# Kernel optimization log

Measured on AMD Instinct MI355X. Metric: run time of the kernel, lower is better.

Reference implementation:

```python
import jax, jax.numpy as jnp
import numpy as np

NEG = -1e9  # sentinel for masked/assigned entries (fp32-safe)


def _greedy_max_connect(logits, mask_dec, mask_tgt):
    """Iterative greedy max-connect matching (previous_max_connect_search).

    Each round, every unassigned query row claims its best available target
    column; conflicts on a column are won by the highest-logit row. Winners
    are fixed and removed, and the process repeats until all valid rows are
    matched (or no columns remain). Returns (index [B,Q] int32,
    one_hot [B,Q,T] float, iter count).
    """
    B, Q, T = logits.shape
    valid = mask_dec[:, :, None] & mask_tgt[:, None, :]
    base = jnp.where(valid, logits, NEG)
    col_ids = jnp.arange(T, dtype=jnp.int32)
    row_ids = jnp.arange(Q, dtype=jnp.int32)

    def cond(state):
        row_done, col_done, assigned, index, it = state
        return jnp.logical_and(jnp.any(~row_done), it < Q)

    def body(state):
        row_done, col_done, assigned, index, it = state
        # mask out finished rows / taken columns
        scores = jnp.where(row_done[:, :, None] | col_done[:, None, :], NEG, base)  # [B,Q,T]
        best_val = jnp.max(scores, axis=-1)                      # [B,Q]
        best_col = jnp.argmax(scores, axis=-1).astype(jnp.int32)  # [B,Q]
        claiming = (~row_done) & (best_val > NEG / 2)
        # claim[b,q,t] = best_val if row q claims col t else NEG
        claim = jnp.where(
            claiming[:, :, None] & (best_col[:, :, None] == col_ids[None, None, :]),
            best_val[:, :, None], NEG)                           # [B,Q,T]
        win_row = jnp.argmax(claim, axis=1).astype(jnp.int32)    # [B,T]
        col_hit = jnp.max(claim, axis=1) > NEG / 2               # [B,T]
        row_wins = (claiming
                    & (jnp.take_along_axis(win_row, best_col, axis=1) == row_ids[None, :])
                    & jnp.take_along_axis(col_hit, best_col, axis=1))  # [B,Q]
        index = jnp.where(row_wins, best_col, index)
        assigned = assigned | row_wins
        # rows with no available column left are retired (stuck)
        row_done = row_done | row_wins | (best_val <= NEG / 2)
        col_done = col_done | col_hit
        return row_done, col_done, assigned, index, it + 1

    init = (~mask_dec, ~mask_tgt,
            jnp.zeros((B, Q), bool), jnp.zeros((B, Q), jnp.int32),
            jnp.array(0, jnp.int32))
    row_done, col_done, assigned, index, it = jax.lax.while_loop(cond, body, init)
    one_hot = (assigned[:, :, None]
               & (index[:, :, None] == col_ids[None, None, :])).astype(logits.dtype)
    return index, one_hot, it


def setup_inputs() -> dict:
    key = jax.random.key(0)
    k1, k2 = jax.random.split(key)
    B, Q, T, D = 4, 2048, 2048, 512
    return {
        "dec": jax.random.normal(k1, (B, Q, D), jnp.float32),
        "tgt": jax.random.normal(k2, (B, T, D), jnp.float32),
        "mask_dec": jnp.ones((B, Q), dtype=bool),
        "mask_tgt": jnp.ones((B, T), dtype=bool),
    }


def reference(dec, tgt, mask_dec, mask_tgt):
    # search_type=0, decompose=False -> inputs = dec, targets = tgt
    # normalize=True -> cosine-style logits (note: torch uses plain norm, no eps)
    inputs = dec / jnp.linalg.norm(dec, axis=-1, keepdims=True)
    targets = tgt / jnp.linalg.norm(tgt, axis=-1, keepdims=True)
    logits = jnp.einsum("bqd,btd->bqt", inputs, targets)  # [B,Q,T]
    index, one_hot, iters = _greedy_max_connect(logits, mask_dec, mask_tgt)
    return logits, index, one_hot, iters
```

## Files before the change

kernel.cpp:

```cpp
#include <hip/hip_runtime.h>

#define B_ 4
#define Q_ 2048
#define T_ 2048
#define D_ 512
#define K_ 16

typedef __attribute__((ext_vector_type(8))) __bf16 bf16x8;
typedef __attribute__((ext_vector_type(4))) float f32x4;

__device__ inline unsigned int fmap(float v) {
  unsigned int b = __float_as_uint(v);
  return (b & 0x80000000u) ? ~b : (b | 0x80000000u);
}

__device__ inline unsigned long long shfl_xor64(unsigned long long v, int m) {
  int lo = __shfl_xor((int)(unsigned int)(v & 0xFFFFFFFFULL), m, 64);
  int hi = __shfl_xor((int)(unsigned int)(v >> 32), m, 64);
  return ((unsigned long long)(unsigned int)hi << 32) | (unsigned int)lo;
}

__global__ __launch_bounds__(256) void convert_kernel(const float* __restrict__ dec,
                                                      const float* __restrict__ tgt,
                                                      __bf16* __restrict__ planes,
                                                      float* __restrict__ rq,
                                                      float* __restrict__ rt,
                                                      int* __restrict__ g_iters) {
  if (blockIdx.x == 0 && threadIdx.x == 0) g_iters[0] = 0;
  const int NR = B_ * Q_;
  int w = (blockIdx.x * blockDim.x + threadIdx.x) >> 6;
  int lane = threadIdx.x & 63;
  const bool isA = (w < NR);
  const int row = isA ? w : w - NR;
  const float* src = (isA ? dec : tgt) + (size_t)row * D_;

  float4 u = *(const float4*)(src + lane * 8);
  float4 v = *(const float4*)(src + lane * 8 + 4);
  float xs[8] = {u.x, u.y, u.z, u.w, v.x, v.y, v.z, v.w};

  bf16x8 h0, h1, h2;
  float s = 0.f;
#pragma unroll
  for (int j = 0; j < 8; ++j) {
    float x = xs[j];
    s += x * x;
    __bf16 a0 = (__bf16)x;
    float r1 = x - (float)a0;
    __bf16 a1 = (__bf16)r1;
    float r2 = r1 - (float)a1;
    __bf16 a2 = (__bf16)r2;
    h0[j] = a0; h1[j] = a1; h2[j] = a2;
  }
  const size_t PS = (size_t)NR * D_;
  __bf16* p = planes + (isA ? 0 : 3) * PS + (size_t)row * D_ + lane * 8;
  *(bf16x8*)(p)          = h0;
  *(bf16x8*)(p + PS)     = h1;
  *(bf16x8*)(p + 2 * PS) = h2;

#pragma unroll
  for (int off = 32; off; off >>= 1) s += __shfl_xor(s, off, 64);
  if (lane == 0) {
    float r = 1.0f / sqrtf(s);
    (isA ? rq : rt)[row] = r;
  }
}

__global__ __launch_bounds__(256) void gemm_kernel(const __bf16* __restrict__ planes,
                                                   const float* __restrict__ rq,
                                                   const float* __restrict__ rt,
                                                   float* __restrict__ C) {
  __shared__ __bf16 sA[3][128][40];
  __shared__ __bf16 sB[3][128][40];

  const size_t PS = (size_t)(B_ * Q_) * D_;
  const int bz = blockIdx.z;
  const int qb = blockIdx.y * 128, tb = blockIdx.x * 128;
  const int arow0 = bz * Q_ + qb;
  const int brow0 = bz * T_ + tb;
  const int t = threadIdx.x;
  const int lane = t & 63, wid = t >> 6;
  const int wr = wid >> 1, wc = wid & 1;
  const int fr = lane & 15;
  const int fg = lane >> 4;

  const __bf16* pA[3] = {planes, planes + PS, planes + 2 * PS};
  const __bf16* pB[3] = {planes + 3 * PS, planes + 4 * PS, planes + 5 * PS};

  f32x4 acc[4][4];
#pragma unroll
  for (int i = 0; i < 4; ++i)
#pragma unroll
    for (int j = 0; j < 4; ++j) acc[i][j] = (f32x4){0.f, 0.f, 0.f, 0.f};

  for (int ks = 0; ks < D_ / 32; ++ks) {
    const int k0 = ks * 32;
    __syncthreads();
#pragma unroll
    for (int p = 0; p < 3; ++p) {
#pragma unroll
      for (int i = 0; i < 2; ++i) {
        int c = t + i * 256;
        int row = c >> 2;
        int off = (c & 3) * 8;
        uint4 va = *(const uint4*)(pA[p] + (size_t)(arow0 + row) * D_ + k0 + off);
        *(uint4*)&sA[p][row][off] = va;
        uint4 vb = *(const uint4*)(pB[p] + (size_t)(brow0 + row) * D_ + k0 + off);
        *(uint4*)&sB[p][row][off] = vb;
      }
    }
    __syncthreads();

    bf16x8 bfr[4][3];
#pragma unroll
    for (int nt = 0; nt < 4; ++nt)
#pragma unroll
      for (int p = 0; p < 3; ++p)
        bfr[nt][p] = *(const bf16x8*)&sB[p][wc * 64 + nt * 16 + fr][fg * 8];

#pragma unroll
    for (int mt = 0; mt < 4; ++mt) {
      bf16x8 afr[3];
#pragma unroll
      for (int p = 0; p < 3; ++p)
        afr[p] = *(const bf16x8*)&sA[p][wr * 64 + mt * 16 + fr][fg * 8];
#pragma unroll
      for (int nt = 0; nt < 4; ++nt) {
        f32x4 c = acc[mt][nt];
        c = __builtin_amdgcn_mfma_f32_16x16x32_bf16(afr[0], bfr[nt][0], c, 0, 0, 0);
        c = __builtin_amdgcn_mfma_f32_16x16x32_bf16(afr[0], bfr[nt][1], c, 0, 0, 0);
        c = __builtin_amdgcn_mfma_f32_16x16x32_bf16(afr[1], bfr[nt][0], c, 0, 0, 0);
        c = __builtin_amdgcn_mfma_f32_16x16x32_bf16(afr[0], bfr[nt][2], c, 0, 0, 0);
        c = __builtin_amdgcn_mfma_f32_16x16x32_bf16(afr[1], bfr[nt][1], c, 0, 0, 0);
        c = __builtin_amdgcn_mfma_f32_16x16x32_bf16(afr[2], bfr[nt][0], c, 0, 0, 0);
        acc[mt][nt] = c;
      }
    }
  }

#pragma unroll
  for (int mt = 0; mt < 4; ++mt) {
    int q = qb + wr * 64 + mt * 16 + fg * 4;
    float rq0 = rq[bz * Q_ + q + 0];
    float rq1 = rq[bz * Q_ + q + 1];
    float rq2 = rq[bz * Q_ + q + 2];
    float rq3 = rq[bz * Q_ + q + 3];
#pragma unroll
    for (int nt = 0; nt < 4; ++nt) {
      int tc = tb + wc * 64 + nt * 16 + fr;
      float rtv = rt[bz * T_ + tc];
      float* cp = C + ((size_t)(bz * Q_ + q)) * T_ + tc;
      cp[0]          = acc[mt][nt][0] * rq0 * rtv;
      cp[T_]         = acc[mt][nt][1] * rq1 * rtv;
      cp[2 * (size_t)T_] = acc[mt][nt][2] * rq2 * rtv;
      cp[3 * (size_t)T_] = acc[mt][nt][3] * rq3 * rtv;
    }
  }
}

__global__ __launch_bounds__(256) void topk_kernel(const float* __restrict__ logits,
                                                   unsigned long long* __restrict__ cand) {
  int w = (blockIdx.x * blockDim.x + threadIdx.x) >> 6;
  int lane = threadIdx.x & 63;
  if (w >= B_ * Q_) return;
  const float* lp = logits + (size_t)w * T_;
  const int c0 = lane << 2;

  unsigned int v[32];
#pragma unroll
  for (int j = 0; j < 8; ++j) {
    float4 x = *(const float4*)(lp + j * 256 + c0);
    v[4 * j + 0] = fmap(x.x);
    v[4 * j + 1] = fmap(x.y);
    v[4 * j + 2] = fmap(x.z);
    v[4 * j + 3] = fmap(x.w);
  }

  unsigned int validmask = 0xFFFFFFFFu;
  unsigned int lm = 0u;
  int lj = 0;
#pragma unroll
  for (int j = 0; j < 32; ++j) {
    bool t = v[j] > lm;
    lm = t ? v[j] : lm;
    lj = t ? j : lj;
  }
  int lc = c0 + ((lj >> 2) << 8) + (lj & 3);

  unsigned long long mine = 0ULL;
#pragma unroll 1
  for (int it = 0; it < K_; ++it) {
    unsigned long long key = ((unsigned long long)lm << 32) | (unsigned int)~lc;
    unsigned long long wmax = key;
#pragma unroll
    for (int off = 32; off; off >>= 1) {
      unsigned long long o = shfl_xor64(wmax, off);
      if (o > wmax) wmax = o;
    }
    if (lane == it) mine = wmax;
    if (key == wmax) {
      validmask &= ~(1u << lj);
      lm = 0u; lj = 0;
#pragma unroll
      for (int j = 0; j < 32; ++j) {
        bool ok = (((validmask >> j) & 1u) != 0u) && (v[j] > lm);
        lm = ok ? v[j] : lm;
        lj = ok ? j : lj;
      }
      lc = c0 + ((lj >> 2) << 8) + (lj & 3);
    }
  }
  if (lane < K_) cand[(size_t)w * K_ + lane] = mine;
}

__global__ __launch_bounds__(1024) void match_kernel(const float* __restrict__ logits,
                                                     unsigned long long* __restrict__ cand,
                                                     int* __restrict__ g_index,
                                                     int* __restrict__ g_assigned,
                                                     int* __restrict__ g_iters) {
  __shared__ unsigned long long claim[T_];
  __shared__ unsigned char col_done[T_];
  __shared__ short bestc[Q_];
  __shared__ short queue[Q_];
  __shared__ short freelist[T_];
  __shared__ int qn, nfree_s, live_s;

  const int b = blockIdx.x;
  const int bq0 = b << 11;
  const int tid = threadIdx.x;
  const int lane = tid & 63, wid = tid >> 6;
  const int q0 = tid, q1 = tid + 1024;
  const unsigned long long lmask_lt = (1ULL << lane) - 1ULL;
  const unsigned int tagA = (unsigned int)~(unsigned int)q0;
  const unsigned int tagB = (unsigned int)~(unsigned int)q1;

  for (int i = tid; i < Q_; i += 1024) {
    claim[i] = 0ULL; col_done[i] = 0;
    g_index[bq0 + i] = 0; g_assigned[bq0 + i] = 0;
  }
  if (tid == 0) { qn = 0; live_s = Q_; }

  bool doneA = false, doneB = false;
  int cpA = 0, cpB = 0;
  unsigned long long ecA = cand[((size_t)(bq0 + q0)) * K_];
  unsigned long long ecB = cand[((size_t)(bq0 + q1)) * K_];

  int r = 0;
  for (;;) {
    __syncthreads();
    if (*(volatile int*)&live_s == 0 || r >= Q_) break;
    if (tid == 0) nfree_s = 0;

    bool clA = false, clB = false, quA = false, quB = false;
    int mcA = -1, mcB = -1;

    if (!doneA) {
      const unsigned long long* cp = cand + ((size_t)(bq0 + q0)) * K_;
      for (;;) {
        if (cpA >= K_ || ecA == 0ULL) { quA = true; break; }
        int c = (int)~(unsigned int)ecA;
        if (!col_done[c]) {
          mcA = c; clA = true;
          atomicMax(&claim[c], (ecA & 0xFFFFFFFF00000000ULL) | tagA);
          break;
        }
        ++cpA; ecA = (cpA < K_) ? cp[cpA] : 0ULL;
      }
    }
    if (!doneB) {
      const unsigned long long* cp = cand + ((size_t)(bq0 + q1)) * K_;
      for (;;) {
        if (cpB >= K_ || ecB == 0ULL) { quB = true; break; }
        int c = (int)~(unsigned int)ecB;
        if (!col_done[c]) {
          mcB = c; clB = true;
          atomicMax(&claim[c], (ecB & 0xFFFFFFFF00000000ULL) | tagB);
          break;
        }
        ++cpB; ecB = (cpB < K_) ? cp[cpB] : 0ULL;
      }
    }
    {
      unsigned long long mA = __ballot(quA);
      unsigned long long mB = __ballot(quB);
      int cntA = __popcll(mA), cntB = __popcll(mB);
      int base = 0;
      if (lane == 0 && (cntA + cntB)) base = atomicAdd(&qn, cntA + cntB);
      base = __shfl(base, 0, 64);
      if (quA) queue[base + __popcll(mA & lmask_lt)] = (short)q0;
      if (quB) queue[base + cntA + __popcll(mB & lmask_lt)] = (short)q1;
    }
    __syncthreads();

    const int nq = qn;
    if (nq > 0) {
      for (int chunk = wid; chunk < T_ / 64; chunk += 16) {
        int c = (chunk << 6) + lane;
        bool fr = (col_done[c] == 0);
        unsigned long long m = __ballot(fr);
        int cnt = __popcll(m);
        int fb = 0;
        if (lane == 0 && cnt) fb = atomicAdd(&nfree_s, cnt);
        fb = __shfl(fb, 0, 64);
        if (fr) freelist[fb + __popcll(m & lmask_lt)] = (short)c;
      }
      __syncthreads();
      const int nf = nfree_s;
      for (int qi = wid; qi < nq; qi += 16) {
        int q = queue[qi];
        const float* lp = logits + ((size_t)(bq0 + q)) * T_;
        unsigned long long best = 0ULL;
        for (int j = lane; j < nf; j += 64) {
          int c = freelist[j];
          unsigned long long kk = ((unsigned long long)fmap(lp[c]) << 32)
                                | (unsigned int)~c;
          if (kk > best) best = kk;
        }
#pragma unroll
        for (int off = 32; off; off >>= 1) {
          unsigned long long o = shfl_xor64(best, off);
          if (o > best) best = o;
        }
        if (lane == 0) {
          unsigned long long* crow = cand + ((size_t)(bq0 + q)) * K_;
          if (best) {
            crow[0] = best; crow[1] = 0ULL;
            int c0 = (int)~(unsigned int)best;
            bestc[q] = (short)c0;
            atomicMax(&claim[c0], (best & 0xFFFFFFFF00000000ULL)
                                  | (unsigned int)~(unsigned int)q);
          } else {
            bestc[q] = -1;
          }
        }
      }
      if (tid == 0) qn = 0;
      __syncthreads();
    }

    bool ndA = false, ndB = false;
    if (!doneA) {
      if (quA) {
        int c = bestc[q0];
        if (c < 0) { doneA = true; ndA = true; }
        else if ((unsigned int)claim[c] == tagA) {
          g_index[bq0 + q0] = c; g_assigned[bq0 + q0] = 1;
          doneA = true; ndA = true;
          col_done[c] = 1; claim[c] = 0ULL;
        } else {
          cpA = 0; ecA = cand[((size_t)(bq0 + q0)) * K_];
        }
      } else if (clA) {
        if ((unsigned int)claim[mcA] == tagA) {
          g_index[bq0 + q0] = mcA; g_assigned[bq0 + q0] = 1;
          doneA = true; ndA = true;
          col_done[mcA] = 1; claim[mcA] = 0ULL;
        }
      }
    }
    if (!doneB) {
      if (quB) {
        int c = bestc[q1];
        if (c < 0) { doneB = true; ndB = true; }
        else if ((unsigned int)claim[c] == tagB) {
          g_index[bq0 + q1] = c; g_assigned[bq0 + q1] = 1;
          doneB = true; ndB = true;
          col_done[c] = 1; claim[c] = 0ULL;
        } else {
          cpB = 0; ecB = cand[((size_t)(bq0 + q1)) * K_];
        }
      } else if (clB) {
        if ((unsigned int)claim[mcB] == tagB) {
          g_index[bq0 + q1] = mcB; g_assigned[bq0 + q1] = 1;
          doneB = true; ndB = true;
          col_done[mcB] = 1; claim[mcB] = 0ULL;
        }
      }
    }
    {
      unsigned long long d1 = __ballot(ndA);
      unsigned long long d2 = __ballot(ndB);
      if (lane == 0) {
        int d = __popcll(d1) + __popcll(d2);
        if (d) atomicSub(&live_s, d);
      }
    }
    ++r;
  }
  if (tid == 0) atomicMax(g_iters, r);
}

__global__ __launch_bounds__(256) void finalize_kernel(const int* __restrict__ g_index,
                                                       const int* __restrict__ g_assigned,
                                                       const int* __restrict__ g_iters,
                                                       float* __restrict__ out_index,
                                                       float* __restrict__ out_onehot,
                                                       float* __restrict__ out_iters) {
  const int gsz = gridDim.x * blockDim.x;
  const int gtid = blockIdx.x * blockDim.x + threadIdx.x;
  for (int i = gtid; i < B_ * Q_; i += gsz) out_index[i] = (float)g_index[i];
  if (gtid == 0) out_iters[0] = (float)g_iters[0];
  const long long NF4 = (long long)B_ * Q_ * T_ / 4;
  for (long long i4 = gtid; i4 < NF4; i4 += gsz) {
    int row = (int)(i4 >> 9);
    int c0 = ((int)i4 & 511) * 4;
    int idx = g_assigned[row] ? g_index[row] : -1;
    float4 v;
    v.x = (c0 + 0 == idx) ? 1.f : 0.f;
    v.y = (c0 + 1 == idx) ? 1.f : 0.f;
    v.z = (c0 + 2 == idx) ? 1.f : 0.f;
    v.w = (c0 + 3 == idx) ? 1.f : 0.f;
    *(float4*)(out_onehot + i4 * 4) = v;
  }
}

extern "C" void kernel_launch(void* const* d_in, const int* in_sizes, int n_in,
                              void* d_out, int out_size, void* d_ws, size_t ws_size,
                              hipStream_t stream) {
  (void)in_sizes; (void)n_in; (void)out_size; (void)ws_size;
  const float* dec = (const float*)d_in[0];
  const float* tgt = (const float*)d_in[1];

  float* out = (float*)d_out;
  float* logits    = out;
  float* out_index = out + (size_t)B_ * Q_ * T_;
  float* out_oh    = out_index + (size_t)B_ * Q_;
  float* out_iters = out_oh + (size_t)B_ * Q_ * T_;

  unsigned long long* cand = (unsigned long long*)out_oh;
  __bf16* planes = (__bf16*)((char*)out_oh + (4u << 20));

  unsigned char* ws = (unsigned char*)d_ws;
  int* g_index    = (int*)ws;
  int* g_assigned = (int*)(ws + 32768);
  int* g_iters    = (int*)(ws + 65536);
  float* rq       = (float*)(ws + 65600);
  float* rt       = rq + B_ * Q_;

  convert_kernel<<<dim3((B_ * Q_ + B_ * T_) / 4), dim3(256), 0, stream>>>(
      dec, tgt, planes, rq, rt, g_iters);
  gemm_kernel<<<dim3(T_ / 128, Q_ / 128, B_), dim3(256), 0, stream>>>(
      planes, rq, rt, logits);
  topk_kernel<<<dim3(B_ * Q_ / 4), dim3(256), 0, stream>>>(logits, cand);
  match_kernel<<<dim3(B_), dim3(1024), 0, stream>>>(logits, cand,
                                                    g_index, g_assigned, g_iters);
  finalize_kernel<<<dim3(1024), dim3(256), 0, stream>>>(g_index, g_assigned, g_iters,
                                                        out_index, out_oh, out_iters);
}
```

Measured before the change: 245.1 us.

## Use direct global-to-LDS loads with XOR swizzle and block remap in GEMM

The GEMM tile loads now use global_load_lds to write straight from global memory into shared memory, skipping the register round trip. The padded shared layout becomes an unpadded one with an XOR swizzle on the 16-byte chunk index, which keeps LDS fragment reads free of bank conflicts. The grid is flattened to 1D and blocks are remapped so that neighbouring blocks, likely spread across XCDs, share the same batch and tiles for better L2 reuse. The risk is that the swizzle and LDS address mapping must exactly match the per-wave layout that the direct LDS load writes.

```diff
diff --git a/kernel.cpp b/kernel.cpp
--- a/kernel.cpp
+++ b/kernel.cpp
@@ -18,6 +18,12 @@
   int lo = __shfl_xor((int)(unsigned int)(v & 0xFFFFFFFFULL), m, 64);
   int hi = __shfl_xor((int)(unsigned int)(v >> 32), m, 64);
   return ((unsigned long long)(unsigned int)hi << 32) | (unsigned int)lo;
+}
+
+__device__ inline void gload_lds16(const void* g, void* l) {
+  __builtin_amdgcn_global_load_lds(
+      (const __attribute__((address_space(1))) void*)g,
+      (__attribute__((address_space(3))) void*)l, 16, 0, 0);
 }
 
 __global__ __launch_bounds__(256) void convert_kernel(const float* __restrict__ dec,
@@ -69,19 +75,26 @@
                                                    const float* __restrict__ rq,
                                                    const float* __restrict__ rt,
                                                    float* __restrict__ C) {
-  __shared__ __bf16 sA[3][128][40];
-  __shared__ __bf16 sB[3][128][40];
+  __shared__ __align__(16) __bf16 sA[3][128][32];
+  __shared__ __align__(16) __bf16 sB[3][128][32];
+
+  const int bid = blockIdx.x;
+  const int swz = (bid & 7) * 128 + (bid >> 3);
+  const int bz = swz >> 8;
+  const int by = (swz >> 4) & 15;
+  const int bx = swz & 15;
 
   const size_t PS = (size_t)(B_ * Q_) * D_;
-  const int bz = blockIdx.z;
-  const int qb = blockIdx.y * 128, tb = blockIdx.x * 128;
+  const int qb = by * 128, tb = bx * 128;
   const int arow0 = bz * Q_ + qb;
   const int brow0 = bz * T_ + tb;
   const int t = threadIdx.x;
-  const int lane = t & 63, wid = t >> 6;
+  const int lane = t & 63;
+  const int wid = t >> 6;
   const int wr = wid >> 1, wc = wid & 1;
   const int fr = lane & 15;
   const int fg = lane >> 4;
+  const int swzfr = (fr >> 1) & 3;
 
   const __bf16* pA[3] = {planes, planes + PS, planes + 2 * PS};
   const __bf16* pB[3] = {planes + 3 * PS, planes + 4 * PS, planes + 5 * PS};
@@ -96,16 +109,18 @@
     const int k0 = ks * 32;
     __syncthreads();
 #pragma unroll
-    for (int p = 0; p < 3; ++p) {
-#pragma unroll
-      for (int i = 0; i < 2; ++i) {
-        int c = t + i * 256;
-        int row = c >> 2;
-        int off = (c & 3) * 8;
-        uint4 va = *(const uint4*)(pA[p] + (size_t)(arow0 + row) * D_ + k0 + off);
-        *(uint4*)&sA[p][row][off] = va;
-        uint4 vb = *(const uint4*)(pB[p] + (size_t)(brow0 + row) * D_ + k0 + off);
-        *(uint4*)&sB[p][row][off] = vb;
+    for (int i = 0; i < 2; ++i) {
+      const int c = t + i * 256;
+      const int row = c >> 2;
+      const int sl = (c & 3) ^ ((row >> 1) & 3);
+      const size_t goff = (size_t)row * D_ + k0 + sl * 8;
+      const int lbyte = (((t >> 6) << 6) + (i << 8)) * 16;
+#pragma unroll
+      for (int p = 0; p < 3; ++p) {
+        gload_lds16(pA[p] + (size_t)arow0 * D_ + goff,
+                    (char*)(&sA[p][0][0]) + lbyte);
+        gload_lds16(pB[p] + (size_t)brow0 * D_ + goff,
+                    (char*)(&sB[p][0][0]) + lbyte);
       }
     }
     __syncthreads();
@@ -115,14 +130,14 @@
     for (int nt = 0; nt < 4; ++nt)
 #pragma unroll
       for (int p = 0; p < 3; ++p)
-        bfr[nt][p] = *(const bf16x8*)&sB[p][wc * 64 + nt * 16 + fr][fg * 8];
+        bfr[nt][p] = *(const bf16x8*)&sB[p][wc * 64 + nt * 16 + fr][(fg ^ swzfr) * 8];
 
 #pragma unroll
     for (int mt = 0; mt < 4; ++mt) {
       bf16x8 afr[3];
 #pragma unroll
       for (int p = 0; p < 3; ++p)
-        afr[p] = *(const bf16x8*)&sA[p][wr * 64 + mt * 16 + fr][fg * 8];
+        afr[p] = *(const bf16x8*)&sA[p][wr * 64 + mt * 16 + fr][(fg ^ swzfr) * 8];
 #pragma unroll
       for (int nt = 0; nt < 4; ++nt) {
         f32x4 c = acc[mt][nt];
@@ -149,8 +164,8 @@
       int tc = tb + wc * 64 + nt * 16 + fr;
       float rtv = rt[bz * T_ + tc];
       float* cp = C + ((size_t)(bz * Q_ + q)) * T_ + tc;
-      cp[0]          = acc[mt][nt][0] * rq0 * rtv;
-      cp[T_]         = acc[mt][nt][1] * rq1 * rtv;
+      cp[0]              = acc[mt][nt][0] * rq0 * rtv;
+      cp[T_]             = acc[mt][nt][1] * rq1 * rtv;
       cp[2 * (size_t)T_] = acc[mt][nt][2] * rq2 * rtv;
       cp[3 * (size_t)T_] = acc[mt][nt][3] * rq3 * rtv;
     }
@@ -438,8 +453,7 @@
 
   convert_kernel<<<dim3((B_ * Q_ + B_ * T_) / 4), dim3(256), 0, stream>>>(
       dec, tgt, planes, rq, rt, g_iters);
-  gemm_kernel<<<dim3(T_ / 128, Q_ / 128, B_), dim3(256), 0, stream>>>(
-      planes, rq, rt, logits);
+  gemm_kernel<<<dim3(1024), dim3(256), 0, stream>>>(planes, rq, rt, logits);
   topk_kernel<<<dim3(B_ * Q_ / 4), dim3(256), 0, stream>>>(logits, cand);
   match_kernel<<<dim3(B_), dim3(1024), 0, stream>>>(logits, cand,
                                                     g_index, g_assigned, g_iters);
```

New measurement: 234.8 us. -4.2%, faster.
